# Kernel tuning notes

Hardware: AMD Instinct MI355X
Metric: run time of the kernel (lower is better)

The kernel has to match this reference:

```python
import jax, jax.numpy as jnp
import numpy as np
import math

B, S = 2, 2048
V, D, H, L, DFF = 1024, 512, 8, 6, 2048
DK = D // H
EPS = 1e-5


def _pos_encoding(seq_len, d_model, dtype):
    pos = jnp.arange(seq_len, dtype=jnp.float32)[:, None]
    div = jnp.exp(jnp.arange(0, d_model, 2, dtype=jnp.float32) * (-math.log(10000.0) / d_model))
    pe = jnp.zeros((seq_len, d_model), dtype=jnp.float32)
    pe = pe.at[:, 0::2].set(jnp.sin(pos * div))
    pe = pe.at[:, 1::2].set(jnp.cos(pos * div))
    return pe.astype(dtype)


def _layernorm(x, w, b):
    mu = jnp.mean(x, axis=-1, keepdims=True)
    var = jnp.mean(jnp.square(x - mu), axis=-1, keepdims=True)
    return (x - mu) * jax.lax.rsqrt(var + EPS) * w + b


def setup_inputs() -> dict:
    key = jax.random.key(0)
    ks = jax.random.split(key, 20)
    s = 0.02
    inp = {
        "input_ids": jax.random.randint(ks[0], (B, S), 1, V),
        "emb": jax.random.normal(ks[1], (V, D)) * s,
        # linear weights stored (in, out) so y = x @ W + b
        "wq": jax.random.normal(ks[2], (L, D, D)) * s,
        "bq": jnp.zeros((L, D)),
        "wk": jax.random.normal(ks[3], (L, D, D)) * s,
        "bk": jnp.zeros((L, D)),
        "wv": jax.random.normal(ks[4], (L, D, D)) * s,
        "bv": jnp.zeros((L, D)),
        "wo": jax.random.normal(ks[5], (L, D, D)) * (s / math.sqrt(2 * L)),
        "bo": jnp.zeros((L, D)),
        "ln1_w": jnp.ones((L, D)), "ln1_b": jnp.zeros((L, D)),
        "ln2_w": jnp.ones((L, D)), "ln2_b": jnp.zeros((L, D)),
        "w1": jax.random.normal(ks[6], (L, D, DFF)) * s,
        "b1": jnp.zeros((L, DFF)),
        "w2": jax.random.normal(ks[7], (L, DFF, D)) * (s / math.sqrt(2 * L)),
        "b2": jnp.zeros((L, D)),
        "out_w": jax.random.normal(ks[8], (D, V)) * s,
        "out_b": jnp.zeros((V,)),
    }
    return inp


def reference(input_ids, emb, wq, bq, wk, bk, wv, bv, wo, bo,
              ln1_w, ln1_b, ln2_w, ln2_b, w1, b1, w2, b2, out_w, out_b):
    pad_mask = (input_ids != 0)                              # [B,S] attend where True
    x = emb[input_ids]                                       # [B,S,D]
    x = x + _pos_encoding(S, D, x.dtype)[None, :, :]
    causal = jnp.tril(jnp.ones((S, S), dtype=bool))          # [S,S]
    mask = causal[None, None, :, :] & pad_mask[:, None, None, :]  # [B,1,S,S]
    scale = 1.0 / math.sqrt(DK)
    for l in range(L):
        h = _layernorm(x, ln1_w[l], ln1_b[l])
        q = (h @ wq[l] + bq[l]).reshape(B, S, H, DK)
        k = (h @ wk[l] + bk[l]).reshape(B, S, H, DK)
        v = (h @ wv[l] + bv[l]).reshape(B, S, H, DK)
        scores = jnp.einsum('bqhd,bkhd->bhqk', q, k) * scale
        scores = jnp.where(mask, scores, -jnp.inf)
        attn = jax.nn.softmax(scores, axis=-1)
        o = jnp.einsum('bhqk,bkhd->bqhd', attn, v).reshape(B, S, D)
        x = o @ wo[l] + bo[l]                                # NOTE: no residual on attention (faithful)
        h2 = _layernorm(x, ln2_w[l], ln2_b[l])
        ff = jax.nn.relu(h2 @ w1[l] + b1[l]) @ w2[l] + b2[l]
        x = x + ff
    logits = x @ out_w + out_b                               # [B,S,V]
    return logits
```

## Files before the change

### kernel.cpp

```cpp
#include <hip/hip_runtime.h>
#include <hip/hip_bf16.h>

#define B_ 2
#define S_ 2048
#define V_ 1024
#define D_ 512
#define H_ 8
#define L_ 6
#define DFF_ 2048
#define DK_ 64
#define MROWS (B_*S_)
#define NEGINF (-__builtin_inff())

typedef __hip_bfloat16 bf16;
typedef __bf16 bf16x8 __attribute__((ext_vector_type(8)));
typedef float f32x4 __attribute__((ext_vector_type(4)));
typedef unsigned short us8 __attribute__((ext_vector_type(8)));
typedef unsigned short us2 __attribute__((ext_vector_type(2)));
typedef unsigned short ushort_t;

__device__ __forceinline__ float bf2f(unsigned short u) {
    return __uint_as_float(((unsigned int)u) << 16);
}
__device__ __forceinline__ unsigned short f2b(float x) {
    unsigned int u = __float_as_uint(x);
    return (unsigned short)((u + 0x7FFFu + ((u >> 16) & 1u)) >> 16);
}
__device__ __forceinline__ float ldin(const void* p, size_t i, int bf) {
    return bf ? bf2f(((const unsigned short*)p)[i]) : ((const float*)p)[i];
}

__global__ void detect_kernel(const unsigned int* __restrict__ w, int* __restrict__ flag) {
    if (threadIdx.x == 0) flag[0] = (w[0] == 0x3F800000u) ? 0 : 1;
}

__global__ __launch_bounds__(256) void embed_kernel(const int* __restrict__ ids,
        const void* __restrict__ emb, float* __restrict__ x, const int* __restrict__ dtf)
{
    const int bf = dtf[0];
    int tid = blockIdx.x * 256 + threadIdx.x;
    int d = tid % D_;
    int bs = tid / D_;
    int s = bs % S_;
    int id = ids[bs];
    float e = ldin(emb, (size_t)id * D_ + d, bf);
    int i2 = d & ~1;
    float div = expf((float)i2 * (-9.210340371976184f / (float)D_));
    float ang = (float)s * div;
    float pe = (d & 1) ? cosf(ang) : sinf(ang);
    x[tid] = e + pe;
}

__global__ __launch_bounds__(256) void ln_kernel(const float* __restrict__ x,
        const void* __restrict__ w, const void* __restrict__ b, size_t off,
        unsigned short* __restrict__ out, const int* __restrict__ dtf)
{
    const int bf = dtf[0];
    __shared__ float red[256];
    const int row = blockIdx.x;
    const int tid = threadIdx.x;
    const float* xr = x + (size_t)row * D_;
    float v0 = xr[tid], v1 = xr[tid + 256];
    red[tid] = v0 + v1; __syncthreads();
    for (int s = 128; s > 0; s >>= 1) { if (tid < s) red[tid] += red[tid + s]; __syncthreads(); }
    float mu = red[0] * (1.f / D_); __syncthreads();
    float d0 = v0 - mu, d1 = v1 - mu;
    red[tid] = d0 * d0 + d1 * d1; __syncthreads();
    for (int s = 128; s > 0; s >>= 1) { if (tid < s) red[tid] += red[tid + s]; __syncthreads(); }
    float var = red[0] * (1.f / D_);
    float rstd = rsqrtf(var + 1e-5f);
    unsigned short* orow = out + (size_t)row * D_;
    orow[tid]       = f2b(d0 * rstd * ldin(w, off + tid, bf)       + ldin(b, off + tid, bf));
    orow[tid + 256] = f2b(d1 * rstd * ldin(w, off + tid + 256, bf) + ldin(b, off + tid + 256, bf));
}

__device__ __forceinline__ void tr_tile(const void* src, size_t off, int K, int N,
        unsigned short* dst, int k0, int n0, int bf, unsigned short (*T)[72])
{
    const int t = threadIdx.x;
    const int r = t >> 2, c = (t & 3) * 16;
    size_t e = off + (size_t)(k0 + r) * N + n0 + c;
    us8 u0, u1;
    if (bf) {
        u0 = *(const us8*)((const unsigned short*)src + e);
        u1 = *(const us8*)((const unsigned short*)src + e + 8);
    } else {
        const float* p = (const float*)src + e;
        float4 f0 = *(const float4*)p, f1 = *(const float4*)(p + 4);
        float4 f2 = *(const float4*)(p + 8), f3 = *(const float4*)(p + 12);
        u0[0]=f2b(f0.x); u0[1]=f2b(f0.y); u0[2]=f2b(f0.z); u0[3]=f2b(f0.w);
        u0[4]=f2b(f1.x); u0[5]=f2b(f1.y); u0[6]=f2b(f1.z); u0[7]=f2b(f1.w);
        u1[0]=f2b(f2.x); u1[1]=f2b(f2.y); u1[2]=f2b(f2.z); u1[3]=f2b(f2.w);
        u1[4]=f2b(f3.x); u1[5]=f2b(f3.y); u1[6]=f2b(f3.z); u1[7]=f2b(f3.w);
    }
    *(us8*)&T[r][c] = u0;
    *(us8*)&T[r][c + 8] = u1;
    __syncthreads();
    us8 o0, o1;
    #pragma unroll
    for (int i = 0; i < 8; ++i) { o0[i] = T[c + i][r]; o1[i] = T[c + 8 + i][r]; }
    *(us8*)&dst[(size_t)(n0 + r) * K + k0 + c] = o0;
    *(us8*)&dst[(size_t)(n0 + r) * K + k0 + c + 8] = o1;
}

__global__ __launch_bounds__(256) void transpose_layer(
        const void* wq, const void* wk, const void* wv, const void* wo,
        const void* w1, const void* w2, size_t offQ, size_t offF,
        unsigned short* twq, unsigned short* twk, unsigned short* twv, unsigned short* two,
        unsigned short* tw1, unsigned short* tw2, const int* __restrict__ dtf)
{
    __shared__ __align__(16) unsigned short T[64][72];
    const int bf = dtf[0];
    int bx = blockIdx.x;
    if (bx < 256) {
        int sel = bx >> 6, tile = bx & 63;
        const void* s = sel == 0 ? wq : sel == 1 ? wk : sel == 2 ? wv : wo;
        unsigned short* d = sel == 0 ? twq : sel == 1 ? twk : sel == 2 ? twv : two;
        tr_tile(s, offQ, D_, D_, d, (tile & 7) * 64, (tile >> 3) * 64, bf, T);
    } else if (bx < 512) {
        int tile = bx - 256;
        tr_tile(w1, offF, D_, DFF_, tw1, (tile & 7) * 64, (tile >> 3) * 64, bf, T);
    } else {
        int tile = bx - 512;
        tr_tile(w2, offF, DFF_, D_, tw2, (tile & 31) * 64, (tile >> 5) * 64, bf, T);
    }
}

__global__ __launch_bounds__(256) void transpose_one(const void* src, size_t off,
        int K, int N, unsigned short* dst, const int* __restrict__ dtf)
{
    __shared__ __align__(16) unsigned short T[64][72];
    int tile = blockIdx.x;
    int tk = K / 64;
    tr_tile(src, off, K, N, dst, (tile % tk) * 64, (tile / tk) * 64, dtf[0], T);
}

template<bool ABF16, int OUTM, bool RELU, bool ADD>
__device__ __forceinline__ void gemm_core64(
        const void* __restrict__ A, const unsigned short* __restrict__ Wt,
        const void* __restrict__ bias, size_t bOff, const float* __restrict__ Res,
        void* __restrict__ Cout, int M, int N, int K, int bf)
{
    __shared__ __align__(16) unsigned short At[64][72];
    __shared__ __align__(16) unsigned short Bt[64][72];
    const int tid = threadIdx.x;
    const int wave = tid >> 6, lane = tid & 63;
    const int quad = lane >> 4, l16 = lane & 15;
    const int wm = (wave >> 1) * 32, wn = (wave & 1) * 32;
    const int n0 = blockIdx.x * 64, m0 = blockIdx.y * 64;
    const int r = tid >> 2, cb = tid & 3;

    f32x4 acc[2][2];
    #pragma unroll
    for (int mt = 0; mt < 2; ++mt)
        #pragma unroll
        for (int nt = 0; nt < 2; ++nt)
            acc[mt][nt] = (f32x4){0.f, 0.f, 0.f, 0.f};

    us8 aR[2], wR[2];
    float4 aF[4];

    auto loadT = [&](int k0) {
        if (ABF16) {
            const unsigned short* Ap = (const unsigned short*)A + (size_t)(m0 + r) * K + k0;
            aR[0] = *(const us8*)(Ap + cb * 8);
            aR[1] = *(const us8*)(Ap + (cb + 4) * 8);
        } else {
            const float* Ap = (const float*)A + (size_t)(m0 + r) * K + k0;
            aF[0] = *(const float4*)(Ap + cb * 8);
            aF[1] = *(const float4*)(Ap + cb * 8 + 4);
            aF[2] = *(const float4*)(Ap + (cb + 4) * 8);
            aF[3] = *(const float4*)(Ap + (cb + 4) * 8 + 4);
        }
        const unsigned short* Wp = Wt + (size_t)(n0 + r) * K + k0;
        wR[0] = *(const us8*)(Wp + cb * 8);
        wR[1] = *(const us8*)(Wp + (cb + 4) * 8);
    };
    auto storeT = [&]() {
        if (ABF16) {
            *(us8*)&At[r][cb * 8] = aR[0];
            *(us8*)&At[r][(cb + 4) * 8] = aR[1];
        } else {
            us8 u0, u1;
            u0[0]=f2b(aF[0].x); u0[1]=f2b(aF[0].y); u0[2]=f2b(aF[0].z); u0[3]=f2b(aF[0].w);
            u0[4]=f2b(aF[1].x); u0[5]=f2b(aF[1].y); u0[6]=f2b(aF[1].z); u0[7]=f2b(aF[1].w);
            u1[0]=f2b(aF[2].x); u1[1]=f2b(aF[2].y); u1[2]=f2b(aF[2].z); u1[3]=f2b(aF[2].w);
            u1[4]=f2b(aF[3].x); u1[5]=f2b(aF[3].y); u1[6]=f2b(aF[3].z); u1[7]=f2b(aF[3].w);
            *(us8*)&At[r][cb * 8] = u0;
            *(us8*)&At[r][(cb + 4) * 8] = u1;
        }
        *(us8*)&Bt[r][cb * 8] = wR[0];
        *(us8*)&Bt[r][(cb + 4) * 8] = wR[1];
    };

    loadT(0);
    for (int k0 = 0; k0 < K; k0 += 64) {
        __syncthreads();
        storeT();
        __syncthreads();
        if (k0 + 64 < K) loadT(k0 + 64);
        bf16x8 af[2][2], bw[2][2];
        #pragma unroll
        for (int mt = 0; mt < 2; ++mt)
            #pragma unroll
            for (int kh = 0; kh < 2; ++kh)
                af[mt][kh] = *(const bf16x8*)&At[wm + mt * 16 + l16][kh * 32 + quad * 8];
        #pragma unroll
        for (int nt = 0; nt < 2; ++nt)
            #pragma unroll
            for (int kh = 0; kh < 2; ++kh)
                bw[nt][kh] = *(const bf16x8*)&Bt[wn + nt * 16 + l16][kh * 32 + quad * 8];
        #pragma unroll
        for (int mt = 0; mt < 2; ++mt)
            #pragma unroll
            for (int nt = 0; nt < 2; ++nt) {
                acc[mt][nt] = __builtin_amdgcn_mfma_f32_16x16x32_bf16(af[mt][0], bw[nt][0], acc[mt][nt], 0, 0, 0);
                acc[mt][nt] = __builtin_amdgcn_mfma_f32_16x16x32_bf16(af[mt][1], bw[nt][1], acc[mt][nt], 0, 0, 0);
            }
    }

    #pragma unroll
    for (int mt = 0; mt < 2; ++mt) {
        #pragma unroll
        for (int nt = 0; nt < 2; ++nt) {
            int col = n0 + wn + nt * 16 + l16;
            float bv = ldin(bias, bOff + col, bf);
            #pragma unroll
            for (int rr = 0; rr < 4; ++rr) {
                int row = m0 + wm + mt * 16 + quad * 4 + rr;
                float c = acc[mt][nt][rr] + bv;
                if (ADD) c += Res[(size_t)row * N + col];
                if (RELU) c = fmaxf(c, 0.f);
                if (OUTM == 0)      ((float*)Cout)[(size_t)row * N + col] = c;
                else if (OUTM == 1) ((unsigned short*)Cout)[(size_t)row * N + col] = f2b(c);
                else {
                    if (bf) ((unsigned short*)Cout)[(size_t)row * N + col] = f2b(c);
                    else    ((float*)Cout)[(size_t)row * N + col] = c;
                }
            }
        }
    }
}

template<bool ABF16, int OUTM, bool RELU, bool ADD>
__global__ __launch_bounds__(256) void gemm64(
        const void* __restrict__ A, const unsigned short* __restrict__ Wt,
        const void* __restrict__ bias, size_t bOff, const float* __restrict__ Res,
        void* __restrict__ Cout, int M, int N, int K, const int* __restrict__ dtf)
{
    gemm_core64<ABF16, OUTM, RELU, ADD>(A, Wt, bias, bOff, Res, Cout, M, N, K, dtf[0]);
}

__global__ __launch_bounds__(256) void gemm_qkv64(
        const unsigned short* __restrict__ h,
        const unsigned short* twq, const unsigned short* twk, const unsigned short* twv,
        const void* bq, const void* bk, const void* bv, size_t bOff,
        unsigned short* q, unsigned short* k, unsigned short* v,
        const int* __restrict__ dtf)
{
    const int z = blockIdx.z;
    const unsigned short* W = (z == 0) ? twq : (z == 1) ? twk : twv;
    const void* bias = (z == 0) ? bq : (z == 1) ? bk : bv;
    unsigned short* out = (z == 0) ? q : (z == 1) ? k : v;
    gemm_core64<true, 1, false, false>(h, W, bias, bOff, nullptr, out, MROWS, D_, D_, dtf[0]);
}

__global__ __launch_bounds__(256) void attn_flash_mfma(
        const unsigned short* __restrict__ qb, const unsigned short* __restrict__ kb,
        const unsigned short* __restrict__ vb, const int* __restrict__ ids,
        unsigned short* __restrict__ ob)
{
    __shared__ __align__(16) unsigned short Qs[64][72];
    __shared__ __align__(16) unsigned short Ks[64][72];
    __shared__ __align__(16) unsigned short Vt[64][72];
    __shared__ __align__(16) unsigned short Ps[64][72];
    __shared__ float msk[64];
    const int tid = threadIdx.x;
    const int wave = tid >> 6, lane = tid & 63;
    const int quad = lane >> 4, l16 = lane & 15;
    const int qt = blockIdx.x, h = blockIdx.y, b = blockIdx.z;
    const size_t hb = (size_t)b * S_ * D_ + (size_t)h * DK_;
    const int sr = tid >> 2, scq = (tid & 3) * 16;
    const int pr = tid >> 3, cv = (tid & 7) * 8;

    {
        const unsigned short* qp = qb + hb + (size_t)(qt * 64 + sr) * D_ + scq;
        *(us8*)&Qs[sr][scq]     = *(const us8*)qp;
        *(us8*)&Qs[sr][scq + 8] = *(const us8*)(qp + 8);
    }

    f32x4 Oa[4];
    float m[4], l[4];
    #pragma unroll
    for (int r = 0; r < 4; ++r) { m[r] = NEGINF; l[r] = 0.f; }
    #pragma unroll
    for (int dt = 0; dt < 4; ++dt) Oa[dt] = (f32x4){0.f, 0.f, 0.f, 0.f};

    for (int kt = 0; kt <= qt; ++kt) {
        __syncthreads();
        {
            const unsigned short* kp = kb + hb + (size_t)(kt * 64 + sr) * D_ + scq;
            *(us8*)&Ks[sr][scq]     = *(const us8*)kp;
            *(us8*)&Ks[sr][scq + 8] = *(const us8*)(kp + 8);
        }
        {
            const unsigned short* vp = vb + hb + (size_t)(kt * 64 + 2 * pr) * D_ + cv;
            us8 va = *(const us8*)vp;
            us8 vb8 = *(const us8*)(vp + D_);
            #pragma unroll
            for (int i = 0; i < 8; ++i) {
                us2 u2 = {va[i], vb8[i]};
                *(us2*)&Vt[cv + i][2 * pr] = u2;
            }
        }
        if (tid < 64) msk[tid] = (ids[b * S_ + kt * 64 + tid] == 0) ? NEGINF : 0.f;
        __syncthreads();

        f32x4 sa[4];
        #pragma unroll
        for (int nt = 0; nt < 4; ++nt) sa[nt] = (f32x4){0.f, 0.f, 0.f, 0.f};
        #pragma unroll
        for (int ks = 0; ks < 2; ++ks) {
            bf16x8 aq = *(const bf16x8*)&Qs[wave * 16 + l16][ks * 32 + quad * 8];
            #pragma unroll
            for (int nt = 0; nt < 4; ++nt) {
                bf16x8 bk = *(const bf16x8*)&Ks[nt * 16 + l16][ks * 32 + quad * 8];
                sa[nt] = __builtin_amdgcn_mfma_f32_16x16x32_bf16(aq, bk, sa[nt], 0, 0, 0);
            }
        }

        #pragma unroll
        for (int r = 0; r < 4; ++r) {
            float sv[4];
            #pragma unroll
            for (int nt = 0; nt < 4; ++nt) {
                float s = sa[nt][r] * 0.125f + msk[nt * 16 + l16];
                if (kt == qt && (nt * 16 + l16) > (wave * 16 + quad * 4 + r)) s = NEGINF;
                sv[nt] = s;
            }
            float rmax = fmaxf(fmaxf(sv[0], sv[1]), fmaxf(sv[2], sv[3]));
            #pragma unroll
            for (int off = 8; off > 0; off >>= 1)
                rmax = fmaxf(rmax, __shfl_xor(rmax, off, 16));
            float mnew = fmaxf(m[r], rmax);
            float alpha = __expf(m[r] - mnew);
            float p[4];
            float rsum = 0.f;
            #pragma unroll
            for (int nt = 0; nt < 4; ++nt) { p[nt] = __expf(sv[nt] - mnew); rsum += p[nt]; }
            #pragma unroll
            for (int off = 8; off > 0; off >>= 1)
                rsum += __shfl_xor(rsum, off, 16);
            l[r] = l[r] * alpha + rsum;
            m[r] = mnew;
            #pragma unroll
            for (int dt = 0; dt < 4; ++dt) Oa[dt][r] *= alpha;
            int prow = wave * 16 + quad * 4 + r;
            #pragma unroll
            for (int nt = 0; nt < 4; ++nt)
                Ps[prow][nt * 16 + l16] = f2b(p[nt]);
        }

        #pragma unroll
        for (int ks = 0; ks < 2; ++ks) {
            bf16x8 ap = *(const bf16x8*)&Ps[wave * 16 + l16][ks * 32 + quad * 8];
            #pragma unroll
            for (int dt = 0; dt < 4; ++dt) {
                bf16x8 bv = *(const bf16x8*)&Vt[dt * 16 + l16][ks * 32 + quad * 8];
                Oa[dt] = __builtin_amdgcn_mfma_f32_16x16x32_bf16(ap, bv, Oa[dt], 0, 0, 0);
            }
        }
    }

    #pragma unroll
    for (int r = 0; r < 4; ++r) {
        float inv = 1.f / l[r];
        int row = qt * 64 + wave * 16 + quad * 4 + r;
        #pragma unroll
        for (int dt = 0; dt < 4; ++dt)
            ob[hb + (size_t)row * D_ + dt * 16 + l16] = f2b(Oa[dt][r] * inv);
    }
}

extern "C" void kernel_launch(void* const* d_in, const int* in_sizes, int n_in,
                              void* d_out, int out_size, void* d_ws, size_t ws_size,
                              hipStream_t stream)
{
    const int* ids  = (const int*)d_in[0];
    const void* emb = d_in[1];
    const void* wq  = d_in[2];
    const void* bq  = d_in[3];
    const void* wk  = d_in[4];
    const void* bk  = d_in[5];
    const void* wv  = d_in[6];
    const void* bv  = d_in[7];
    const void* wo  = d_in[8];
    const void* bo  = d_in[9];
    const void* ln1w = d_in[10];
    const void* ln1b = d_in[11];
    const void* ln2w = d_in[12];
    const void* ln2b = d_in[13];
    const void* w1  = d_in[14];
    const void* b1  = d_in[15];
    const void* w2  = d_in[16];
    const void* b2  = d_in[17];
    const void* outw = d_in[18];
    const void* outb = d_in[19];

    char* wsp = (char*)d_ws;
    int* dtf = (int*)wsp;
    const size_t NROW = (size_t)MROWS * D_;
    float* xA = (float*)(wsp + 256);
    float* xB = xA + NROW;
    unsigned short* h  = (unsigned short*)(xB + NROW);
    unsigned short* q  = h + NROW;
    unsigned short* k  = q + NROW;
    unsigned short* v  = k + NROW;
    unsigned short* o  = v + NROW;
    unsigned short* ff = o + NROW;
    unsigned short* twq = ff + (size_t)MROWS * DFF_;
    unsigned short* twk = twq + D_ * D_;
    unsigned short* twv = twk + D_ * D_;
    unsigned short* two = twv + D_ * D_;
    unsigned short* tw1 = two + D_ * D_;
    unsigned short* tw2 = tw1 + (size_t)D_ * DFF_;
    unsigned short* twout = tw2 + (size_t)D_ * DFF_;

    detect_kernel<<<1, 64, 0, stream>>>((const unsigned int*)ln1w, dtf);
    embed_kernel<<<(MROWS * D_) / 256, 256, 0, stream>>>(ids, emb, xA, dtf);
    transpose_one<<<(D_/64) * (V_/64), 256, 0, stream>>>(outw, 0, D_, V_, twout, dtf);

    for (int l = 0; l < L_; ++l) {
        const size_t offQ = (size_t)l * D_ * D_;
        const size_t offF = (size_t)l * D_ * DFF_;
        const size_t bOff = (size_t)l * D_;
        transpose_layer<<<768, 256, 0, stream>>>(wq, wk, wv, wo, w1, w2, offQ, offF,
                                                 twq, twk, twv, two, tw1, tw2, dtf);
        ln_kernel<<<MROWS, 256, 0, stream>>>(xA, ln1w, ln1b, bOff, h, dtf);
        gemm_qkv64<<<dim3(D_/64, MROWS/64, 3), 256, 0, stream>>>(
            h, twq, twk, twv, bq, bk, bv, bOff, q, k, v, dtf);
        attn_flash_mfma<<<dim3(S_/64, H_, B_), 256, 0, stream>>>(q, k, v, ids, o);
        gemm64<true, 0, false, false><<<dim3(D_/64, MROWS/64), 256, 0, stream>>>(
            o, two, bo, bOff, nullptr, xB, MROWS, D_, D_, dtf);
        ln_kernel<<<MROWS, 256, 0, stream>>>(xB, ln2w, ln2b, bOff, h, dtf);
        gemm64<true, 1, true, false><<<dim3(DFF_/64, MROWS/64), 256, 0, stream>>>(
            h, tw1, b1, (size_t)l * DFF_, nullptr, ff, MROWS, DFF_, D_, dtf);
        gemm64<true, 0, false, true><<<dim3(D_/64, MROWS/64), 256, 0, stream>>>(
            ff, tw2, b2, bOff, xB, xA, MROWS, D_, DFF_, dtf);
    }
    gemm64<false, 2, false, false><<<dim3(V_/64, MROWS/64), 256, 0, stream>>>(
        xA, twout, outb, 0, nullptr, d_out, MROWS, V_, D_, dtf);
}
```

Measured before the change: 1.146 ms.

## Batch weight transposes, pair causal query tiles, double-buffer K/V in attention

Weight transposes for all six layers are done in a single upfront launch when the workspace is large enough, replacing the per-layer transpose kernels. The attention kernel now handles two query tiles per block (qt and 31-qt) to balance the causal triangular work. It also double-buffers K/V in shared memory with register prefetch of the next tile, and preloads the whole padding mask once. This trades more shared memory and workspace for fewer launches, better load balance and overlap of global loads with MFMA work.

```diff
diff --git a/kernel.cpp b/kernel.cpp
--- a/kernel.cpp
+++ b/kernel.cpp
@@ -17,7 +17,6 @@
 typedef float f32x4 __attribute__((ext_vector_type(4)));
 typedef unsigned short us8 __attribute__((ext_vector_type(8)));
 typedef unsigned short us2 __attribute__((ext_vector_type(2)));
-typedef unsigned short ushort_t;
 
 __device__ __forceinline__ float bf2f(unsigned short u) {
     return __uint_as_float(((unsigned int)u) << 16);
@@ -103,26 +102,34 @@
     *(us8*)&dst[(size_t)(n0 + r) * K + k0 + c + 8] = o1;
 }
 
-__global__ __launch_bounds__(256) void transpose_layer(
+__global__ __launch_bounds__(256) void transpose_all(
         const void* wq, const void* wk, const void* wv, const void* wo,
-        const void* w1, const void* w2, size_t offQ, size_t offF,
+        const void* w1, const void* w2,
         unsigned short* twq, unsigned short* twk, unsigned short* twv, unsigned short* two,
-        unsigned short* tw1, unsigned short* tw2, const int* __restrict__ dtf)
+        unsigned short* tw1, unsigned short* tw2,
+        int lbase, int slotmul, const int* __restrict__ dtf)
 {
     __shared__ __align__(16) unsigned short T[64][72];
     const int bf = dtf[0];
-    int bx = blockIdx.x;
-    if (bx < 256) {
-        int sel = bx >> 6, tile = bx & 63;
+    const int lrel = blockIdx.x / 768;
+    const int within = blockIdx.x % 768;
+    const int layer = lbase + lrel;
+    const int slot = lrel * slotmul;
+    const size_t offQ = (size_t)layer * D_ * D_;
+    const size_t offF = (size_t)layer * D_ * DFF_;
+    const size_t sQ = (size_t)slot * D_ * D_;
+    const size_t sF = (size_t)slot * D_ * DFF_;
+    if (within < 256) {
+        int sel = within >> 6, tile = within & 63;
         const void* s = sel == 0 ? wq : sel == 1 ? wk : sel == 2 ? wv : wo;
-        unsigned short* d = sel == 0 ? twq : sel == 1 ? twk : sel == 2 ? twv : two;
+        unsigned short* d = (sel == 0 ? twq : sel == 1 ? twk : sel == 2 ? twv : two) + sQ;
         tr_tile(s, offQ, D_, D_, d, (tile & 7) * 64, (tile >> 3) * 64, bf, T);
-    } else if (bx < 512) {
-        int tile = bx - 256;
-        tr_tile(w1, offF, D_, DFF_, tw1, (tile & 7) * 64, (tile >> 3) * 64, bf, T);
+    } else if (within < 512) {
+        int tile = within - 256;
+        tr_tile(w1, offF, D_, DFF_, tw1 + sF, (tile & 7) * 64, (tile >> 3) * 64, bf, T);
     } else {
-        int tile = bx - 512;
-        tr_tile(w2, offF, DFF_, D_, tw2, (tile & 31) * 64, (tile >> 5) * 64, bf, T);
+        int tile = within - 512;
+        tr_tile(w2, offF, DFF_, D_, tw2 + sF, (tile & 31) * 64, (tile >> 5) * 64, bf, T);
     }
 }
 
@@ -265,120 +272,138 @@
     gemm_core64<true, 1, false, false>(h, W, bias, bOff, nullptr, out, MROWS, D_, D_, dtf[0]);
 }
 
-__global__ __launch_bounds__(256) void attn_flash_mfma(
+__global__ __launch_bounds__(256) void attn_flash_v3(
         const unsigned short* __restrict__ qb, const unsigned short* __restrict__ kb,
         const unsigned short* __restrict__ vb, const int* __restrict__ ids,
         unsigned short* __restrict__ ob)
 {
     __shared__ __align__(16) unsigned short Qs[64][72];
-    __shared__ __align__(16) unsigned short Ks[64][72];
-    __shared__ __align__(16) unsigned short Vt[64][72];
+    __shared__ __align__(16) unsigned short Ks[2][64][72];
+    __shared__ __align__(16) unsigned short Vt[2][64][72];
     __shared__ __align__(16) unsigned short Ps[64][72];
-    __shared__ float msk[64];
+    __shared__ float Msk[S_];
     const int tid = threadIdx.x;
     const int wave = tid >> 6, lane = tid & 63;
     const int quad = lane >> 4, l16 = lane & 15;
-    const int qt = blockIdx.x, h = blockIdx.y, b = blockIdx.z;
+    const int pidx = blockIdx.x, h = blockIdx.y, b = blockIdx.z;
     const size_t hb = (size_t)b * S_ * D_ + (size_t)h * DK_;
     const int sr = tid >> 2, scq = (tid & 3) * 16;
-    const int pr = tid >> 3, cv = (tid & 7) * 8;
-
-    {
-        const unsigned short* qp = qb + hb + (size_t)(qt * 64 + sr) * D_ + scq;
-        *(us8*)&Qs[sr][scq]     = *(const us8*)qp;
-        *(us8*)&Qs[sr][scq + 8] = *(const us8*)(qp + 8);
-    }
-
-    f32x4 Oa[4];
-    float m[4], l[4];
-    #pragma unroll
-    for (int r = 0; r < 4; ++r) { m[r] = NEGINF; l[r] = 0.f; }
-    #pragma unroll
-    for (int dt = 0; dt < 4; ++dt) Oa[dt] = (f32x4){0.f, 0.f, 0.f, 0.f};
-
-    for (int kt = 0; kt <= qt; ++kt) {
+    const int pr = tid >> 3, cvb = tid & 7;
+
+    for (int i = tid; i < S_; i += 256)
+        Msk[i] = (ids[b * S_ + i] == 0) ? NEGINF : 0.f;
+
+    us8 kR0, kR1, vA, vB;
+    auto loadKV = [&](int kt) {
+        const unsigned short* kp = kb + hb + (size_t)(kt * 64 + sr) * D_ + scq;
+        kR0 = *(const us8*)kp;
+        kR1 = *(const us8*)(kp + 8);
+        const unsigned short* vp = vb + hb + (size_t)(kt * 64 + 2 * pr) * D_ + cvb * 8;
+        vA = *(const us8*)vp;
+        vB = *(const us8*)(vp + D_);
+    };
+    auto storeKV = [&](int buf) {
+        *(us8*)&Ks[buf][sr][scq]     = kR0;
+        *(us8*)&Ks[buf][sr][scq + 8] = kR1;
+        #pragma unroll
+        for (int i = 0; i < 8; ++i) {
+            int ii = (i + cvb) & 7;
+            us2 u2 = { vA[ii], vB[ii] };
+            *(us2*)&Vt[buf][cvb * 8 + ii][2 * pr] = u2;
+        }
+    };
+
+    const int qts[2] = { pidx, 31 - pidx };
+    #pragma unroll 1
+    for (int pass = 0; pass < 2; ++pass) {
+        const int qt = qts[pass];
         __syncthreads();
         {
-            const unsigned short* kp = kb + hb + (size_t)(kt * 64 + sr) * D_ + scq;
-            *(us8*)&Ks[sr][scq]     = *(const us8*)kp;
-            *(us8*)&Ks[sr][scq + 8] = *(const us8*)(kp + 8);
-        }
-        {
-            const unsigned short* vp = vb + hb + (size_t)(kt * 64 + 2 * pr) * D_ + cv;
-            us8 va = *(const us8*)vp;
-            us8 vb8 = *(const us8*)(vp + D_);
-            #pragma unroll
-            for (int i = 0; i < 8; ++i) {
-                us2 u2 = {va[i], vb8[i]};
-                *(us2*)&Vt[cv + i][2 * pr] = u2;
-            }
-        }
-        if (tid < 64) msk[tid] = (ids[b * S_ + kt * 64 + tid] == 0) ? NEGINF : 0.f;
+            const unsigned short* qp = qb + hb + (size_t)(qt * 64 + sr) * D_ + scq;
+            *(us8*)&Qs[sr][scq]     = *(const us8*)qp;
+            *(us8*)&Qs[sr][scq + 8] = *(const us8*)(qp + 8);
+        }
+        f32x4 Oa[4];
+        float m[4], l[4];
+        #pragma unroll
+        for (int r = 0; r < 4; ++r) { m[r] = NEGINF; l[r] = 0.f; }
+        #pragma unroll
+        for (int dt = 0; dt < 4; ++dt) Oa[dt] = (f32x4){0.f, 0.f, 0.f, 0.f};
+
+        loadKV(0);
+        storeKV(0);
+        if (qt >= 1) loadKV(1);
         __syncthreads();
 
-        f32x4 sa[4];
-        #pragma unroll
-        for (int nt = 0; nt < 4; ++nt) sa[nt] = (f32x4){0.f, 0.f, 0.f, 0.f};
-        #pragma unroll
-        for (int ks = 0; ks < 2; ++ks) {
-            bf16x8 aq = *(const bf16x8*)&Qs[wave * 16 + l16][ks * 32 + quad * 8];
-            #pragma unroll
-            for (int nt = 0; nt < 4; ++nt) {
-                bf16x8 bk = *(const bf16x8*)&Ks[nt * 16 + l16][ks * 32 + quad * 8];
-                sa[nt] = __builtin_amdgcn_mfma_f32_16x16x32_bf16(aq, bk, sa[nt], 0, 0, 0);
-            }
-        }
-
+        #pragma unroll 1
+        for (int kt = 0; kt <= qt; ++kt) {
+            const int cur = kt & 1;
+            f32x4 sa[4];
+            #pragma unroll
+            for (int nt = 0; nt < 4; ++nt) sa[nt] = (f32x4){0.f, 0.f, 0.f, 0.f};
+            #pragma unroll
+            for (int ks = 0; ks < 2; ++ks) {
+                bf16x8 aq = *(const bf16x8*)&Qs[wave * 16 + l16][ks * 32 + quad * 8];
+                #pragma unroll
+                for (int nt = 0; nt < 4; ++nt) {
+                    bf16x8 bk = *(const bf16x8*)&Ks[cur][nt * 16 + l16][ks * 32 + quad * 8];
+                    sa[nt] = __builtin_amdgcn_mfma_f32_16x16x32_bf16(aq, bk, sa[nt], 0, 0, 0);
+                }
+            }
+            #pragma unroll
+            for (int r = 0; r < 4; ++r) {
+                float sv[4];
+                #pragma unroll
+                for (int nt = 0; nt < 4; ++nt) {
+                    float s = sa[nt][r] * 0.125f + Msk[kt * 64 + nt * 16 + l16];
+                    if (kt == qt && (nt * 16 + l16) > (wave * 16 + quad * 4 + r)) s = NEGINF;
+                    sv[nt] = s;
+                }
+                float rmax = fmaxf(fmaxf(sv[0], sv[1]), fmaxf(sv[2], sv[3]));
+                #pragma unroll
+                for (int off = 8; off > 0; off >>= 1)
+                    rmax = fmaxf(rmax, __shfl_xor(rmax, off, 16));
+                float mnew = fmaxf(m[r], rmax);
+                float alpha = __expf(m[r] - mnew);
+                float p[4];
+                float rsum = 0.f;
+                #pragma unroll
+                for (int nt = 0; nt < 4; ++nt) { p[nt] = __expf(sv[nt] - mnew); rsum += p[nt]; }
+                #pragma unroll
+                for (int off = 8; off > 0; off >>= 1)
+                    rsum += __shfl_xor(rsum, off, 16);
+                l[r] = l[r] * alpha + rsum;
+                m[r] = mnew;
+                #pragma unroll
+                for (int dt = 0; dt < 4; ++dt) Oa[dt][r] *= alpha;
+                int prow = wave * 16 + quad * 4 + r;
+                #pragma unroll
+                for (int nt = 0; nt < 4; ++nt)
+                    Ps[prow][nt * 16 + l16] = f2b(p[nt]);
+            }
+            #pragma unroll
+            for (int ks = 0; ks < 2; ++ks) {
+                bf16x8 ap = *(const bf16x8*)&Ps[wave * 16 + l16][ks * 32 + quad * 8];
+                #pragma unroll
+                for (int dt = 0; dt < 4; ++dt) {
+                    bf16x8 bv = *(const bf16x8*)&Vt[cur][dt * 16 + l16][ks * 32 + quad * 8];
+                    Oa[dt] = __builtin_amdgcn_mfma_f32_16x16x32_bf16(ap, bv, Oa[dt], 0, 0, 0);
+                }
+            }
+            if (kt + 1 <= qt) {
+                storeKV(cur ^ 1);
+                if (kt + 2 <= qt) loadKV(kt + 2);
+                __syncthreads();
+            }
+        }
         #pragma unroll
         for (int r = 0; r < 4; ++r) {
-            float sv[4];
-            #pragma unroll
-            for (int nt = 0; nt < 4; ++nt) {
-                float s = sa[nt][r] * 0.125f + msk[nt * 16 + l16];
-                if (kt == qt && (nt * 16 + l16) > (wave * 16 + quad * 4 + r)) s = NEGINF;
-                sv[nt] = s;
-            }
-            float rmax = fmaxf(fmaxf(sv[0], sv[1]), fmaxf(sv[2], sv[3]));
-            #pragma unroll
-            for (int off = 8; off > 0; off >>= 1)
-                rmax = fmaxf(rmax, __shfl_xor(rmax, off, 16));
-            float mnew = fmaxf(m[r], rmax);
-            float alpha = __expf(m[r] - mnew);
-            float p[4];
-            float rsum = 0.f;
-            #pragma unroll
-            for (int nt = 0; nt < 4; ++nt) { p[nt] = __expf(sv[nt] - mnew); rsum += p[nt]; }
-            #pragma unroll
-            for (int off = 8; off > 0; off >>= 1)
-                rsum += __shfl_xor(rsum, off, 16);
-            l[r] = l[r] * alpha + rsum;
-            m[r] = mnew;
-            #pragma unroll
-            for (int dt = 0; dt < 4; ++dt) Oa[dt][r] *= alpha;
-            int prow = wave * 16 + quad * 4 + r;
-            #pragma unroll
-            for (int nt = 0; nt < 4; ++nt)
-                Ps[prow][nt * 16 + l16] = f2b(p[nt]);
-        }
-
-        #pragma unroll
-        for (int ks = 0; ks < 2; ++ks) {
-            bf16x8 ap = *(const bf16x8*)&Ps[wave * 16 + l16][ks * 32 + quad * 8];
-            #pragma unroll
-            for (int dt = 0; dt < 4; ++dt) {
-                bf16x8 bv = *(const bf16x8*)&Vt[dt * 16 + l16][ks * 32 + quad * 8];
-                Oa[dt] = __builtin_amdgcn_mfma_f32_16x16x32_bf16(ap, bv, Oa[dt], 0, 0, 0);
-            }
-        }
-    }
-
-    #pragma unroll
-    for (int r = 0; r < 4; ++r) {
-        float inv = 1.f / l[r];
-        int row = qt * 64 + wave * 16 + quad * 4 + r;
-        #pragma unroll
-        for (int dt = 0; dt < 4; ++dt)
-            ob[hb + (size_t)row * D_ + dt * 16 + l16] = f2b(Oa[dt][r] * inv);
+            float inv = 1.f / l[r];
+            int row = qt * 64 + wave * 16 + quad * 4 + r;
+            #pragma unroll
+            for (int dt = 0; dt < 4; ++dt)
+                ob[hb + (size_t)row * D_ + dt * 16 + l16] = f2b(Oa[dt][r] * inv);
+        }
     }
 }
 
@@ -410,6 +435,15 @@
     char* wsp = (char*)d_ws;
     int* dtf = (int*)wsp;
     const size_t NROW = (size_t)MROWS * D_;
+
+    const size_t fixedBytes = 256
+        + 2 * NROW * 4
+        + 5 * NROW * 2
+        + (size_t)MROWS * DFF_ * 2
+        + (size_t)D_ * V_ * 2;
+    const size_t perLayerW = (4 * (size_t)D_ * D_ + 2 * (size_t)D_ * DFF_) * 2;
+    const int slots = (ws_size >= fixedBytes + 6 * perLayerW) ? 6 : 1;
+
     float* xA = (float*)(wsp + 256);
     float* xB = xA + NROW;
     unsigned short* h  = (unsigned short*)(xB + NROW);
@@ -418,35 +452,45 @@
     unsigned short* v  = k + NROW;
     unsigned short* o  = v + NROW;
     unsigned short* ff = o + NROW;
-    unsigned short* twq = ff + (size_t)MROWS * DFF_;
-    unsigned short* twk = twq + D_ * D_;
-    unsigned short* twv = twk + D_ * D_;
-    unsigned short* two = twv + D_ * D_;
-    unsigned short* tw1 = two + D_ * D_;
-    unsigned short* tw2 = tw1 + (size_t)D_ * DFF_;
-    unsigned short* twout = tw2 + (size_t)D_ * DFF_;
+    unsigned short* twout = ff + (size_t)MROWS * DFF_;
+    unsigned short* twq = twout + (size_t)D_ * V_;
+    unsigned short* twk = twq + (size_t)slots * D_ * D_;
+    unsigned short* twv = twk + (size_t)slots * D_ * D_;
+    unsigned short* two = twv + (size_t)slots * D_ * D_;
+    unsigned short* tw1 = two + (size_t)slots * D_ * D_;
+    unsigned short* tw2 = tw1 + (size_t)slots * D_ * DFF_;
 
     detect_kernel<<<1, 64, 0, stream>>>((const unsigned int*)ln1w, dtf);
+    transpose_one<<<(D_/64) * (V_/64), 256, 0, stream>>>(outw, 0, D_, V_, twout, dtf);
+    if (slots == 6)
+        transpose_all<<<6 * 768, 256, 0, stream>>>(wq, wk, wv, wo, w1, w2,
+            twq, twk, twv, two, tw1, tw2, 0, 1, dtf);
     embed_kernel<<<(MROWS * D_) / 256, 256, 0, stream>>>(ids, emb, xA, dtf);
-    transpose_one<<<(D_/64) * (V_/64), 256, 0, stream>>>(outw, 0, D_, V_, twout, dtf);
 
     for (int l = 0; l < L_; ++l) {
-        const size_t offQ = (size_t)l * D_ * D_;
-        const size_t offF = (size_t)l * D_ * DFF_;
         const size_t bOff = (size_t)l * D_;
-        transpose_layer<<<768, 256, 0, stream>>>(wq, wk, wv, wo, w1, w2, offQ, offF,
-                                                 twq, twk, twv, two, tw1, tw2, dtf);
+        const int s = (slots == 6) ? l : 0;
+        if (slots == 1)
+            transpose_all<<<768, 256, 0, stream>>>(wq, wk, wv, wo, w1, w2,
+                twq, twk, twv, two, tw1, tw2, l, 0, dtf);
+        const unsigned short* lwq = twq + (size_t)s * D_ * D_;
+        const unsigned short* lwk = twk + (size_t)s * D_ * D_;
+        const unsigned short* lwv = twv + (size_t)s * D_ * D_;
+        const unsigned short* lwo = two + (size_t)s * D_ * D_;
+        const unsigned short* lw1 = tw1 + (size_t)s * D_ * DFF_;
+        const unsigned short* lw2 = tw2 + (size_t)s * D_ * DFF_;
+
         ln_kernel<<<MROWS, 256, 0, stream>>>(xA, ln1w, ln1b, bOff, h, dtf);
         gemm_qkv64<<<dim3(D_/64, MROWS/64, 3), 256, 0, stream>>>(
-            h, twq, twk, twv, bq, bk, bv, bOff, q, k, v, dtf);
-        attn_flash_mfma<<<dim3(S_/64, H_, B_), 256, 0, stream>>>(q, k, v, ids, o);
+            h, lwq, lwk, lwv, bq, bk, bv, bOff, q, k, v, dtf);
+        attn_flash_v3<<<dim3(S_/128, H_, B_), 256, 0, stream>>>(q, k, v, ids, o);
         gemm64<true, 0, false, false><<<dim3(D_/64, MROWS/64), 256, 0, stream>>>(
-            o, two, bo, bOff, nullptr, xB, MROWS, D_, D_, dtf);
+            o, lwo, bo, bOff, nullptr, xB, MROWS, D_, D_, dtf);
         ln_kernel<<<MROWS, 256, 0, stream>>>(xB, ln2w, ln2b, bOff, h, dtf);
         gemm64<true, 1, true, false><<<dim3(DFF_/64, MROWS/64), 256, 0, stream>>>(
-            h, tw1, b1, (size_t)l * DFF_, nullptr, ff, MROWS, DFF_, D_, dtf);
+            h, lw1, b1, (size_t)l * DFF_, nullptr, ff, MROWS, DFF_, D_, dtf);
         gemm64<true, 0, false, true><<<dim3(D_/64, MROWS/64), 256, 0, stream>>>(
-            ff, tw2, b2, bOff, xB, xA, MROWS, D_, DFF_, dtf);
+            ff, lw2, b2, bOff, xB, xA, MROWS, D_, DFF_, dtf);
     }
     gemm64<false, 2, false, false><<<dim3(V_/64, MROWS/64), 256, 0, stream>>>(
         xA, twout, outb, 0, nullptr, d_out, MROWS, V_, D_, dtf);
```

Result: faster. 1.047 ms (-8.6%).
